# Kernel optimization log

Measured on AMD Instinct MI355X. Metric: run time of the kernel, lower is better.

Reference implementation:

```python
import jax, jax.numpy as jnp
import numpy as np

N = 50000      # nodes
DEG = 16       # fixed neighbor count per node -> E = N*DEG edges
F_IN = 128
F_OUT = 128


def setup_inputs() -> dict:
    key = jax.random.key(0)
    k = jax.random.split(key, 6)
    E = N * DEG
    x = jax.random.normal(k[0], (N, F_IN), dtype=jnp.float32)
    weight = jax.random.normal(k[1], (F_IN, F_OUT), dtype=jnp.float32) * (1.0 / np.sqrt(F_OUT))
    bias = jax.random.normal(k[2], (F_OUT,), dtype=jnp.float32) * (1.0 / np.sqrt(F_OUT))
    weights_mask = jax.random.normal(k[3], (2 * F_IN, F_IN), dtype=jnp.float32) * (1.0 / np.sqrt(F_IN))
    adj_vals = jax.random.uniform(k[4], (E,), dtype=jnp.float32)
    edge_src = jax.random.randint(k[5], (E,), 0, N, dtype=jnp.int32)   # neighbor ids (add_all flattened)
    edge_dst = jnp.repeat(jnp.arange(N, dtype=jnp.int32), DEG)         # center node ids
    return {"x": x, "weight": weight, "bias": bias, "weights_mask": weights_mask,
            "adj_vals": adj_vals, "edge_src": edge_src, "edge_dst": edge_dst}


def reference(x, weight, bias, weights_mask, adj_vals, edge_src, edge_dst):
    # Per-edge: concat(center, neighbor) -> mask MLP -> sigmoid (dropout omitted: eval mode)
    cen = x[edge_dst]                    # [E, F]
    nei = x[edge_src]                    # [E, F]
    cen_nei = jnp.concatenate([cen, nei], axis=1)          # [E, 2F]
    mask = jax.nn.sigmoid(cen_nei @ weights_mask)          # [E, F]
    # Weighted neighbor sum scattered back to centers, plus self feature
    agg = jax.ops.segment_sum(mask * nei, edge_dst, num_segments=N)   # [N, F]
    x_new = x + agg
    # Dense transform then spmm aggregation (adj given as edge list with values)
    support = x_new @ weight                                # [N, F_out]
    out = jax.ops.segment_sum(adj_vals[:, None] * support[edge_src], edge_dst, num_segments=N)
    return out + bias
```

## Files before the change

### kernel.cpp

```cpp
#include <hip/hip_runtime.h>
#include <stdint.h>
#include <stddef.h>


#define NNODES 50000
#define DEG    16
#define FD     128

#define NEG_LOG2E -1.44269504f

typedef __bf16 bf16x8 __attribute__((ext_vector_type(8)));
typedef short  s16x8  __attribute__((ext_vector_type(8)));
typedef float  f32x4  __attribute__((ext_vector_type(4)));
typedef float  f32x2  __attribute__((ext_vector_type(2)));

__device__ __forceinline__ short f2bf_s(float f) {
    union { float f; uint32_t u; } v; v.f = f;
    uint32_t r = v.u + 0x7fffu + ((v.u >> 16) & 1u);
    return (short)(r >> 16);
}
__device__ __forceinline__ float bflo(uint32_t u) {
    union { uint32_t u; float f; } v; v.u = u << 16;
    return v.f;
}
__device__ __forceinline__ float bfhi(uint32_t u) {
    union { uint32_t u; float f; } v; v.u = u & 0xffff0000u;
    return v.f;
}

__global__ __launch_bounds__(256) void pack_k(const float* __restrict__ wm,
                                              const float* __restrict__ w,
                                              short* __restrict__ wmb,
                                              short* __restrict__ wpack) {
    int tid = blockIdx.x * 256 + threadIdx.x;
    if (tid < 128 * 256) {
        int k = tid >> 8, c = tid & 255;
        float v = (c < 128) ? wm[k * 128 + c] : wm[(128 + k) * 128 + (c - 128)];
        int idx = (((k >> 5) * 16 + (c >> 4)) * 64 + ((k >> 3) & 3) * 16 + (c & 15)) * 8 + (k & 7);
        wmb[idx] = f2bf_s(NEG_LOG2E * v);
    }
    if (tid < 128 * 128) {
        int k = tid >> 7, n = tid & 127;
        int idx = (((k >> 5) * 8 + (n >> 4)) * 64 + ((k >> 3) & 3) * 16 + (n & 15)) * 8 + (k & 7);
        wpack[idx] = f2bf_s(w[tid]);
    }
}

__global__ __launch_bounds__(256) void zy_k(const float* __restrict__ x,
                                            const short* __restrict__ wmb,
                                            short* __restrict__ zbf,
                                            uint32_t* __restrict__ xb,
                                            uint8_t* __restrict__ y8) {
    __shared__ float ct[16 * 260];
    const int tid = threadIdx.x, wave = tid >> 6, lane = tid & 63;
    const int q = lane >> 4, m = lane & 15;
    const int node0 = blockIdx.x * 16;

    f32x4 acc[4];
    #pragma unroll
    for (int nt = 0; nt < 4; ++nt) acc[nt] = (f32x4){0.f, 0.f, 0.f, 0.f};

    #pragma unroll
    for (int kk = 0; kk < 4; ++kk) {
        const float* rp = x + (size_t)(node0 + m) * FD + kk * 32 + q * 8;
        f32x4 lo = *reinterpret_cast<const f32x4*>(rp);
        f32x4 hi = *reinterpret_cast<const f32x4*>(rp + 4);
        bf16x8 a;
        a[0]=(__bf16)lo.x; a[1]=(__bf16)lo.y; a[2]=(__bf16)lo.z; a[3]=(__bf16)lo.w;
        a[4]=(__bf16)hi.x; a[5]=(__bf16)hi.y; a[6]=(__bf16)hi.z; a[7]=(__bf16)hi.w;
        #pragma unroll
        for (int nt = 0; nt < 4; ++nt) {
            int frag = kk * 16 + wave * 4 + nt;
            s16x8 braw = *reinterpret_cast<const s16x8*>(wmb + ((size_t)frag * 64 + lane) * 8);
            acc[nt] = __builtin_amdgcn_mfma_f32_16x16x32_bf16(a, __builtin_bit_cast(bf16x8, braw), acc[nt], 0, 0, 0);
        }
    }
    #pragma unroll
    for (int nt = 0; nt < 4; ++nt)
        #pragma unroll
        for (int i = 0; i < 4; ++i)
            ct[(q * 4 + i) * 260 + wave * 64 + nt * 16 + m] = acc[nt][i];
    __syncthreads();

    const int row = tid >> 4;
    const int c0  = (tid & 15) * 16;
    const int grow = node0 + row;
    if (c0 < 128) {
        uint32_t zo[8];
        #pragma unroll
        for (int j = 0; j < 8; ++j) {
            float v0 = ct[row * 260 + c0 + 2 * j];
            float v1 = ct[row * 260 + c0 + 2 * j + 1];
            zo[j] = (uint32_t)(uint16_t)f2bf_s(v0) | ((uint32_t)(uint16_t)f2bf_s(v1) << 16);
        }
        uint4* dst = reinterpret_cast<uint4*>(zbf + (size_t)grow * FD + c0);
        dst[0] = make_uint4(zo[0], zo[1], zo[2], zo[3]);
        dst[1] = make_uint4(zo[4], zo[5], zo[6], zo[7]);
    } else {
        const int f0 = c0 - 128;
        const float* xr = x + (size_t)grow * FD + f0;
        uint32_t xo[8];
        #pragma unroll
        for (int j = 0; j < 8; ++j) {
            float v0 = xr[2 * j], v1 = xr[2 * j + 1];
            xo[j] = (uint32_t)(uint16_t)f2bf_s(v0) | ((uint32_t)(uint16_t)f2bf_s(v1) << 16);
        }
        uint4* xdst = reinterpret_cast<uint4*>(xb + (size_t)grow * 64 + f0 / 2);
        xdst[0] = make_uint4(xo[0], xo[1], xo[2], xo[3]);
        xdst[1] = make_uint4(xo[4], xo[5], xo[6], xo[7]);
        uint32_t yo[4];
        #pragma unroll
        for (int g = 0; g < 4; ++g) {
            float y0 = ct[row * 260 + c0 + 4 * g];
            float y1 = ct[row * 260 + c0 + 4 * g + 1];
            float y2 = ct[row * 260 + c0 + 4 * g + 2];
            float y3 = ct[row * 260 + c0 + 4 * g + 3];
            int u = __builtin_amdgcn_cvt_pk_fp8_f32(y0, y1, 0, false);
            u     = __builtin_amdgcn_cvt_pk_fp8_f32(y2, y3, u, true);
            yo[g] = (uint32_t)u;
        }
        *reinterpret_cast<uint4*>(y8 + (size_t)grow * 128 + f0) = make_uint4(yo[0], yo[1], yo[2], yo[3]);
    }
}

__global__ __launch_bounds__(256) void edge_k(const short* __restrict__ zbf,
                                              const uint32_t* __restrict__ xb,
                                              const uint8_t* __restrict__ y8,
                                              const int* __restrict__ esrc,
                                              uint32_t* __restrict__ xnb) {
    const int tid = threadIdx.x, wave = tid >> 6, lane = tid & 63;
    const int wn0 = blockIdx.x * 16 + wave * 4;

    #pragma unroll
    for (int pr = 0; pr < 2; ++pr) {
        const int nuA = __builtin_amdgcn_readfirstlane(wn0 + pr * 2);
        const int nuB = __builtin_amdgcn_readfirstlane(wn0 + pr * 2 + 1);
        const int* epA = esrc + nuA * DEG;
        const int* epB = esrc + nuB * DEG;
        uint32_t zA = reinterpret_cast<const uint32_t*>(zbf + (size_t)nuA * FD)[lane];
        uint32_t zB = reinterpret_cast<const uint32_t*>(zbf + (size_t)nuB * FD)[lane];
        uint32_t cAw = xb[(size_t)nuA * 64 + lane];
        uint32_t cBw = xb[(size_t)nuB * 64 + lane];
        const float zA0 = bflo(zA), zA1 = bfhi(zA);
        const float zB0 = bflo(zB), zB1 = bfhi(zB);
        float aA0 = 0.f, aA1 = 0.f, bA0 = 0.f, bA1 = 0.f;
        float aB0 = 0.f, aB1 = 0.f, bB0 = 0.f, bB1 = 0.f;
        #pragma unroll
        for (int e = 0; e < 16; ++e) {
            const int sA = epA[e], sB = epB[e];
            uint32_t xA = xb[(size_t)sA * 64 + lane];
            uint32_t xB = xb[(size_t)sB * 64 + lane];
            uint32_t yA = *reinterpret_cast<const uint16_t*>(y8 + (size_t)sA * 128 + 2 * lane);
            uint32_t yB = *reinterpret_cast<const uint16_t*>(y8 + (size_t)sB * 128 + 2 * lane);
            f32x2 pA = __builtin_amdgcn_cvt_pk_f32_fp8((int)yA, false);
            f32x2 pB = __builtin_amdgcn_cvt_pk_f32_fp8((int)yB, false);
            float gA0 = __builtin_amdgcn_rcpf(1.f + __builtin_amdgcn_exp2f(zA0 + pA.x));
            float gA1 = __builtin_amdgcn_rcpf(1.f + __builtin_amdgcn_exp2f(zA1 + pA.y));
            float gB0 = __builtin_amdgcn_rcpf(1.f + __builtin_amdgcn_exp2f(zB0 + pB.x));
            float gB1 = __builtin_amdgcn_rcpf(1.f + __builtin_amdgcn_exp2f(zB1 + pB.y));
            if (e & 1) { bA0 += gA0 * bflo(xA); bA1 += gA1 * bfhi(xA); bB0 += gB0 * bflo(xB); bB1 += gB1 * bfhi(xB); }
            else       { aA0 += gA0 * bflo(xA); aA1 += gA1 * bfhi(xA); aB0 += gB0 * bflo(xB); aB1 += gB1 * bfhi(xB); }
        }
        float xA0 = bflo(cAw) + aA0 + bA0, xA1 = bfhi(cAw) + aA1 + bA1;
        float xB0 = bflo(cBw) + aB0 + bB0, xB1 = bfhi(cBw) + aB1 + bB1;
        xnb[(size_t)nuA * 64 + lane] = (uint32_t)(uint16_t)f2bf_s(xA0) | ((uint32_t)(uint16_t)f2bf_s(xA1) << 16);
        xnb[(size_t)nuB * 64 + lane] = (uint32_t)(uint16_t)f2bf_s(xB0) | ((uint32_t)(uint16_t)f2bf_s(xB1) << 16);
    }
}

__global__ __launch_bounds__(256) void out_k(const uint32_t* __restrict__ xnb,
                                             const float* __restrict__ adj,
                                             const int* __restrict__ esrc,
                                             const short* __restrict__ wpack,
                                             const float* __restrict__ bias,
                                             float* __restrict__ out) {
    __shared__ float xn[16 * 132];
    const int tid = threadIdx.x, wave = tid >> 6, lane = tid & 63;
    const int q = lane >> 4, m = lane & 15;
    const int node0 = blockIdx.x * 16;
    const int wn0 = node0 + wave * 4;

    #pragma unroll
    for (int pr = 0; pr < 2; ++pr) {
        const int nuA = __builtin_amdgcn_readfirstlane(wn0 + pr * 2);
        const int nuB = __builtin_amdgcn_readfirstlane(wn0 + pr * 2 + 1);
        const int* epA = esrc + nuA * DEG;
        const int* epB = esrc + nuB * DEG;
        const float* apA = adj + nuA * DEG;
        const float* apB = adj + nuB * DEG;
        float aA0 = 0.f, aA1 = 0.f, bA0 = 0.f, bA1 = 0.f;
        float aB0 = 0.f, aB1 = 0.f, bB0 = 0.f, bB1 = 0.f;
        #pragma unroll
        for (int e = 0; e < 16; ++e) {
            uint32_t uA = xnb[(size_t)epA[e] * 64 + lane];
            uint32_t uB = xnb[(size_t)epB[e] * 64 + lane];
            float wA = apA[e], wB = apB[e];
            if (e & 1) { bA0 += wA * bflo(uA); bA1 += wA * bfhi(uA); bB0 += wB * bflo(uB); bB1 += wB * bfhi(uB); }
            else       { aA0 += wA * bflo(uA); aA1 += wA * bfhi(uA); aB0 += wB * bflo(uB); aB1 += wB * bfhi(uB); }
        }
        const int rA = wave * 4 + pr * 2, rB = rA + 1;
        f32x2 tA; tA.x = aA0 + bA0; tA.y = aA1 + bA1;
        f32x2 tB; tB.x = aB0 + bB0; tB.y = aB1 + bB1;
        *reinterpret_cast<f32x2*>(&xn[rA * 132 + 2 * lane]) = tA;
        *reinterpret_cast<f32x2*>(&xn[rB * 132 + 2 * lane]) = tB;
    }
    __syncthreads();

    f32x4 sacc[2];
    sacc[0] = (f32x4){0.f, 0.f, 0.f, 0.f};
    sacc[1] = (f32x4){0.f, 0.f, 0.f, 0.f};
    #pragma unroll
    for (int kk = 0; kk < 4; ++kk) {
        const float* p = &xn[m * 132 + kk * 32 + q * 8];
        bf16x8 a;
        a[0]=(__bf16)p[0]; a[1]=(__bf16)p[1]; a[2]=(__bf16)p[2]; a[3]=(__bf16)p[3];
        a[4]=(__bf16)p[4]; a[5]=(__bf16)p[5]; a[6]=(__bf16)p[6]; a[7]=(__bf16)p[7];
        #pragma unroll
        for (int t = 0; t < 2; ++t) {
            int nt = wave * 2 + t;
            s16x8 braw = *reinterpret_cast<const s16x8*>(wpack + ((size_t)(kk * 8 + nt) * 64 + lane) * 8);
            sacc[t] = __builtin_amdgcn_mfma_f32_16x16x32_bf16(a, __builtin_bit_cast(bf16x8, braw), sacc[t], 0, 0, 0);
        }
    }
    #pragma unroll
    for (int t = 0; t < 2; ++t) {
        const int f = (wave * 2 + t) * 16 + m;
        const float bv = bias[f];
        #pragma unroll
        for (int i = 0; i < 4; ++i)
            out[(size_t)(node0 + q * 4 + i) * FD + f] = sacc[t][i] + bv;
    }
}

extern "C" void kernel_launch(void* const* d_in, const int* in_sizes, int n_in,
                              void* d_out, int out_size, void* d_ws, size_t ws_size,
                              hipStream_t stream) {
    const float* x      = (const float*)d_in[0];
    const float* weight = (const float*)d_in[1];
    const float* bias   = (const float*)d_in[2];
    const float* wm     = (const float*)d_in[3];
    const float* adj    = (const float*)d_in[4];
    const int*   esrc   = (const int*)d_in[5];

    short*    wmb   = (short*)d_ws;
    short*    wpack = (short*)((char*)d_ws + 65536);
    short*    zbf   = (short*)((char*)d_ws + 98304);
    uint32_t* xnb   = (uint32_t*)((char*)d_ws + 98304 + (size_t)NNODES * FD * 2);
    uint32_t* xb    = (uint32_t*)d_out;
    uint8_t*  y8    = (uint8_t*)d_out + (size_t)NNODES * FD * 2;
    float*    out   = (float*)d_out;

    pack_k <<<128,         256, 0, stream>>>(wm, weight, wmb, wpack);
    zy_k   <<<NNODES / 16, 256, 0, stream>>>(x, wmb, zbf, xb, y8);
    edge_k <<<NNODES / 16, 256, 0, stream>>>(zbf, xb, y8, esrc, xnb);
    out_k  <<<NNODES / 16, 256, 0, stream>>>(xnb, adj, esrc, wpack, bias, out);
}
```

Before: 180.3 us.

## Split waves into 16-lane node groups with vectorized gathers and shuffled indices

Edge and output kernels now map each wave to four nodes at once: each 16-lane group owns one node and every lane loads 8 features with 16-byte vector loads. Neighbor indices and adjacency weights are loaded once per wave and broadcast with shuffles, so the per-edge scalar loads go away. The aim is to cut gather instruction count and to have more independent memory requests in flight. In exchange, each lane holds more accumulators and each edge costs a cross-lane shuffle.

```diff
diff --git a/kernel.cpp b/kernel.cpp
--- a/kernel.cpp
+++ b/kernel.cpp
@@ -129,43 +129,49 @@
                                               const int* __restrict__ esrc,
                                               uint32_t* __restrict__ xnb) {
     const int tid = threadIdx.x, wave = tid >> 6, lane = tid & 63;
-    const int wn0 = blockIdx.x * 16 + wave * 4;
-
-    #pragma unroll
-    for (int pr = 0; pr < 2; ++pr) {
-        const int nuA = __builtin_amdgcn_readfirstlane(wn0 + pr * 2);
-        const int nuB = __builtin_amdgcn_readfirstlane(wn0 + pr * 2 + 1);
-        const int* epA = esrc + nuA * DEG;
-        const int* epB = esrc + nuB * DEG;
-        uint32_t zA = reinterpret_cast<const uint32_t*>(zbf + (size_t)nuA * FD)[lane];
-        uint32_t zB = reinterpret_cast<const uint32_t*>(zbf + (size_t)nuB * FD)[lane];
-        uint32_t cAw = xb[(size_t)nuA * 64 + lane];
-        uint32_t cBw = xb[(size_t)nuB * 64 + lane];
-        const float zA0 = bflo(zA), zA1 = bfhi(zA);
-        const float zB0 = bflo(zB), zB1 = bfhi(zB);
-        float aA0 = 0.f, aA1 = 0.f, bA0 = 0.f, bA1 = 0.f;
-        float aB0 = 0.f, aB1 = 0.f, bB0 = 0.f, bB1 = 0.f;
-        #pragma unroll
-        for (int e = 0; e < 16; ++e) {
-            const int sA = epA[e], sB = epB[e];
-            uint32_t xA = xb[(size_t)sA * 64 + lane];
-            uint32_t xB = xb[(size_t)sB * 64 + lane];
-            uint32_t yA = *reinterpret_cast<const uint16_t*>(y8 + (size_t)sA * 128 + 2 * lane);
-            uint32_t yB = *reinterpret_cast<const uint16_t*>(y8 + (size_t)sB * 128 + 2 * lane);
-            f32x2 pA = __builtin_amdgcn_cvt_pk_f32_fp8((int)yA, false);
-            f32x2 pB = __builtin_amdgcn_cvt_pk_f32_fp8((int)yB, false);
-            float gA0 = __builtin_amdgcn_rcpf(1.f + __builtin_amdgcn_exp2f(zA0 + pA.x));
-            float gA1 = __builtin_amdgcn_rcpf(1.f + __builtin_amdgcn_exp2f(zA1 + pA.y));
-            float gB0 = __builtin_amdgcn_rcpf(1.f + __builtin_amdgcn_exp2f(zB0 + pB.x));
-            float gB1 = __builtin_amdgcn_rcpf(1.f + __builtin_amdgcn_exp2f(zB1 + pB.y));
-            if (e & 1) { bA0 += gA0 * bflo(xA); bA1 += gA1 * bfhi(xA); bB0 += gB0 * bflo(xB); bB1 += gB1 * bfhi(xB); }
-            else       { aA0 += gA0 * bflo(xA); aA1 += gA1 * bfhi(xA); aB0 += gB0 * bflo(xB); aB1 += gB1 * bfhi(xB); }
-        }
-        float xA0 = bflo(cAw) + aA0 + bA0, xA1 = bfhi(cAw) + aA1 + bA1;
-        float xB0 = bflo(cBw) + aB0 + bB0, xB1 = bfhi(cBw) + aB1 + bB1;
-        xnb[(size_t)nuA * 64 + lane] = (uint32_t)(uint16_t)f2bf_s(xA0) | ((uint32_t)(uint16_t)f2bf_s(xA1) << 16);
-        xnb[(size_t)nuB * 64 + lane] = (uint32_t)(uint16_t)f2bf_s(xB0) | ((uint32_t)(uint16_t)f2bf_s(xB1) << 16);
-    }
+    const int t = lane & 15;
+    const int node0 = blockIdx.x * 16;
+    const int node = node0 + wave * 4 + (lane >> 4);
+
+    const int idxv = esrc[node0 * DEG + wave * 64 + lane];
+
+    uint4 zw = *reinterpret_cast<const uint4*>(reinterpret_cast<const uint32_t*>(zbf) + (size_t)node * 64 + t * 4);
+    const float z0 = bflo(zw.x), z1 = bfhi(zw.x), z2 = bflo(zw.y), z3 = bfhi(zw.y);
+    const float z4 = bflo(zw.z), z5 = bfhi(zw.z), z6 = bflo(zw.w), z7 = bfhi(zw.w);
+    uint4 cw = *reinterpret_cast<const uint4*>(xb + (size_t)node * 64 + t * 4);
+
+    float acc[8];
+    #pragma unroll
+    for (int j = 0; j < 8; ++j) acc[j] = 0.f;
+
+    #pragma unroll
+    for (int e = 0; e < 16; ++e) {
+        const int s = __shfl(idxv, (lane & 48) + e);
+        uint4 u = *reinterpret_cast<const uint4*>(xb + (size_t)s * 64 + t * 4);
+        uint2 y = *reinterpret_cast<const uint2*>(y8 + (size_t)s * 128 + t * 8);
+        f32x2 p0 = __builtin_amdgcn_cvt_pk_f32_fp8((int)y.x, false);
+        f32x2 p1 = __builtin_amdgcn_cvt_pk_f32_fp8((int)y.x, true);
+        f32x2 p2 = __builtin_amdgcn_cvt_pk_f32_fp8((int)y.y, false);
+        f32x2 p3 = __builtin_amdgcn_cvt_pk_f32_fp8((int)y.y, true);
+        acc[0] += __builtin_amdgcn_rcpf(1.f + __builtin_amdgcn_exp2f(z0 + p0.x)) * bflo(u.x);
+        acc[1] += __builtin_amdgcn_rcpf(1.f + __builtin_amdgcn_exp2f(z1 + p0.y)) * bfhi(u.x);
+        acc[2] += __builtin_amdgcn_rcpf(1.f + __builtin_amdgcn_exp2f(z2 + p1.x)) * bflo(u.y);
+        acc[3] += __builtin_amdgcn_rcpf(1.f + __builtin_amdgcn_exp2f(z3 + p1.y)) * bfhi(u.y);
+        acc[4] += __builtin_amdgcn_rcpf(1.f + __builtin_amdgcn_exp2f(z4 + p2.x)) * bflo(u.z);
+        acc[5] += __builtin_amdgcn_rcpf(1.f + __builtin_amdgcn_exp2f(z5 + p2.y)) * bfhi(u.z);
+        acc[6] += __builtin_amdgcn_rcpf(1.f + __builtin_amdgcn_exp2f(z6 + p3.x)) * bflo(u.w);
+        acc[7] += __builtin_amdgcn_rcpf(1.f + __builtin_amdgcn_exp2f(z7 + p3.y)) * bfhi(u.w);
+    }
+
+    uint32_t cc[4] = {cw.x, cw.y, cw.z, cw.w};
+    uint32_t o[4];
+    #pragma unroll
+    for (int j = 0; j < 4; ++j) {
+        float lo = bflo(cc[j]) + acc[2 * j];
+        float hi = bfhi(cc[j]) + acc[2 * j + 1];
+        o[j] = (uint32_t)(uint16_t)f2bf_s(lo) | ((uint32_t)(uint16_t)f2bf_s(hi) << 16);
+    }
+    *reinterpret_cast<uint4*>(xnb + (size_t)node * 64 + t * 4) = make_uint4(o[0], o[1], o[2], o[3]);
 }
 
 __global__ __launch_bounds__(256) void out_k(const uint32_t* __restrict__ xnb,
@@ -177,32 +183,32 @@
     __shared__ float xn[16 * 132];
     const int tid = threadIdx.x, wave = tid >> 6, lane = tid & 63;
     const int q = lane >> 4, m = lane & 15;
+    const int t = lane & 15;
     const int node0 = blockIdx.x * 16;
-    const int wn0 = node0 + wave * 4;
-
-    #pragma unroll
-    for (int pr = 0; pr < 2; ++pr) {
-        const int nuA = __builtin_amdgcn_readfirstlane(wn0 + pr * 2);
-        const int nuB = __builtin_amdgcn_readfirstlane(wn0 + pr * 2 + 1);
-        const int* epA = esrc + nuA * DEG;
-        const int* epB = esrc + nuB * DEG;
-        const float* apA = adj + nuA * DEG;
-        const float* apB = adj + nuB * DEG;
-        float aA0 = 0.f, aA1 = 0.f, bA0 = 0.f, bA1 = 0.f;
-        float aB0 = 0.f, aB1 = 0.f, bB0 = 0.f, bB1 = 0.f;
-        #pragma unroll
-        for (int e = 0; e < 16; ++e) {
-            uint32_t uA = xnb[(size_t)epA[e] * 64 + lane];
-            uint32_t uB = xnb[(size_t)epB[e] * 64 + lane];
-            float wA = apA[e], wB = apB[e];
-            if (e & 1) { bA0 += wA * bflo(uA); bA1 += wA * bfhi(uA); bB0 += wB * bflo(uB); bB1 += wB * bfhi(uB); }
-            else       { aA0 += wA * bflo(uA); aA1 += wA * bfhi(uA); aB0 += wB * bflo(uB); aB1 += wB * bfhi(uB); }
-        }
-        const int rA = wave * 4 + pr * 2, rB = rA + 1;
-        f32x2 tA; tA.x = aA0 + bA0; tA.y = aA1 + bA1;
-        f32x2 tB; tB.x = aB0 + bB0; tB.y = aB1 + bB1;
-        *reinterpret_cast<f32x2*>(&xn[rA * 132 + 2 * lane]) = tA;
-        *reinterpret_cast<f32x2*>(&xn[rB * 132 + 2 * lane]) = tB;
+
+    const int   idxv = esrc[node0 * DEG + wave * 64 + lane];
+    union { float f; int i; } au; au.f = adj[node0 * DEG + wave * 64 + lane];
+    const int adji = au.i;
+
+    float acc[8];
+    #pragma unroll
+    for (int j = 0; j < 8; ++j) acc[j] = 0.f;
+
+    #pragma unroll
+    for (int e = 0; e < 16; ++e) {
+        const int s = __shfl(idxv, (lane & 48) + e);
+        union { int i; float f; } wu; wu.i = __shfl(adji, (lane & 48) + e);
+        const float w = wu.f;
+        uint4 u = *reinterpret_cast<const uint4*>(xnb + (size_t)s * 64 + t * 4);
+        acc[0] += w * bflo(u.x); acc[1] += w * bfhi(u.x);
+        acc[2] += w * bflo(u.y); acc[3] += w * bfhi(u.y);
+        acc[4] += w * bflo(u.z); acc[5] += w * bfhi(u.z);
+        acc[6] += w * bflo(u.w); acc[7] += w * bfhi(u.w);
+    }
+    {
+        float* dst = &xn[(wave * 4 + (lane >> 4)) * 132 + t * 8];
+        *reinterpret_cast<f32x4*>(dst)     = (f32x4){acc[0], acc[1], acc[2], acc[3]};
+        *reinterpret_cast<f32x4*>(dst + 4) = (f32x4){acc[4], acc[5], acc[6], acc[7]};
     }
     __syncthreads();
 
@@ -216,19 +222,19 @@
         a[0]=(__bf16)p[0]; a[1]=(__bf16)p[1]; a[2]=(__bf16)p[2]; a[3]=(__bf16)p[3];
         a[4]=(__bf16)p[4]; a[5]=(__bf16)p[5]; a[6]=(__bf16)p[6]; a[7]=(__bf16)p[7];
         #pragma unroll
-        for (int t = 0; t < 2; ++t) {
-            int nt = wave * 2 + t;
+        for (int tt = 0; tt < 2; ++tt) {
+            int nt = wave * 2 + tt;
             s16x8 braw = *reinterpret_cast<const s16x8*>(wpack + ((size_t)(kk * 8 + nt) * 64 + lane) * 8);
-            sacc[t] = __builtin_amdgcn_mfma_f32_16x16x32_bf16(a, __builtin_bit_cast(bf16x8, braw), sacc[t], 0, 0, 0);
-        }
-    }
-    #pragma unroll
-    for (int t = 0; t < 2; ++t) {
-        const int f = (wave * 2 + t) * 16 + m;
+            sacc[tt] = __builtin_amdgcn_mfma_f32_16x16x32_bf16(a, __builtin_bit_cast(bf16x8, braw), sacc[tt], 0, 0, 0);
+        }
+    }
+    #pragma unroll
+    for (int tt = 0; tt < 2; ++tt) {
+        const int f = (wave * 2 + tt) * 16 + m;
         const float bv = bias[f];
         #pragma unroll
         for (int i = 0; i < 4; ++i)
-            out[(size_t)(node0 + q * 4 + i) * FD + f] = sacc[t][i] + bv;
+            out[(size_t)(node0 + q * 4 + i) * FD + f] = sacc[tt][i] + bv;
     }
 }
 
```

After: 181.6 us. Within noise of the previous version (+0.7%).
